# Kernel tuning notes

Hardware: AMD Instinct MI355X
Metric: run time of the kernel (lower is better)

## Reference

```python
import jax, jax.numpy as jnp
import numpy as np

DIM = 512
HEADS = 8
HEAD_DIM = DIM // HEADS
LN_EPS = 1e-5


def setup_inputs() -> dict:
    key = jax.random.key(0)
    ks = jax.random.split(key, 16)
    B, L, E = 4, 4096, DIM
    x = jax.random.normal(ks[0], (B, L, E), dtype=jnp.float32)
    w = lambda k: jax.random.normal(k, (E, E), dtype=jnp.float32) * 0.02
    b = lambda k: jax.random.normal(k, (E,), dtype=jnp.float32) * 0.02
    return {
        "x": x,
        "ln_gamma": jnp.ones((E,), jnp.float32),
        "ln_beta": jnp.zeros((E,), jnp.float32),
        "Wqr": w(ks[1]), "bqr": b(ks[2]),
        "Wqi": w(ks[3]), "bqi": b(ks[4]),
        "Wkr": w(ks[5]), "bkr": b(ks[6]),
        "Wki": w(ks[7]), "bki": b(ks[8]),
        "Wvr": w(ks[9]), "bvr": b(ks[10]),
        "Wvi": w(ks[11]), "bvi": b(ks[12]),
        "Wo": w(ks[13]),
    }


def reference(x, ln_gamma, ln_beta, Wqr, bqr, Wqi, bqi, Wkr, bkr, Wki, bki,
              Wvr, bvr, Wvi, bvi, Wo):
    B, L, E = x.shape
    H, d = HEADS, HEAD_DIM
    # LayerNorm over last dim
    mu = jnp.mean(x, axis=-1, keepdims=True)
    var = jnp.mean(jnp.square(x - mu), axis=-1, keepdims=True)
    xn = (x - mu) * jax.lax.rsqrt(var + LN_EPS) * ln_gamma + ln_beta
    # rfft along time dim -> F = L//2 + 1 frequency bins
    xf = jnp.fft.rfft(xn, axis=1, norm="ortho")
    xr, xi = jnp.real(xf), jnp.imag(xf)  # [B, F, E]
    # split real/imag QKV projections (torch Linear: y = x @ W.T + b)
    Qr = xr @ Wqr.T + bqr
    Qi = xi @ Wqi.T + bqi
    Kr = xr @ Wkr.T + bkr
    Ki = xi @ Wki.T + bki
    Vr = xr @ Wvr.T + bvr
    Vi = xi @ Wvi.T + bvi
    Fn = xr.shape[1]
    split = lambda t: t.reshape(B, Fn, H, d)  # b l (h d) -> b l h d
    Qr, Qi, Kr, Ki, Vr, Vi = map(split, (Qr, Qi, Kr, Ki, Vr, Vi))
    # scores = Qr.Kr + Qi.Ki, scaled softmax over keys
    scores = (jnp.einsum("blhd,bmhd->bhlm", Qr, Kr)
              + jnp.einsum("blhd,bmhd->bhlm", Qi, Ki))
    attn = jax.nn.softmax(scores * (d ** -0.5), axis=-1)
    out_r = jnp.einsum("bhlm,bmhd->bhld", attn, Vr)
    out_i = jnp.einsum("bhlm,bmhd->bhld", attn, Vi)
    out_f = jax.lax.complex(out_r, out_i)  # [B, H, F, d]
    out_f = jnp.transpose(out_f, (0, 2, 1, 3)).reshape(B, Fn, E)
    out_t = jnp.fft.irfft(out_f, n=L, axis=1, norm="ortho")
    return out_t @ Wo.T
```

## Files before the change

### kernel.cpp

```cpp
#include <hip/hip_runtime.h>
#include <math.h>

#define NB 4
#define NL 4096
#define NE 512
#define NH 8
#define ND 64
#define NF 2049
#define WSZ (NE * NE)

static constexpr float INV_SQRT_N = 1.0f / 64.0f;

typedef __attribute__((ext_vector_type(8))) short bf16x8;
typedef __attribute__((ext_vector_type(4))) short short4v;
typedef __attribute__((ext_vector_type(4))) float f32x4;

__device__ __forceinline__ float2 cmul(float2 a, float2 b) {
    return make_float2(a.x * b.x - a.y * b.y, a.x * b.y + a.y * b.x);
}

__device__ __forceinline__ short cvt_bf16(float f) {
    unsigned u = __float_as_uint(f);
    unsigned r = (u + 0x7FFFu + ((u >> 16) & 1u)) >> 16;
    return (short)r;
}

__device__ __forceinline__ int pack_bf16x2(float a, float b) {
    return (int)(unsigned short)cvt_bf16(a) | ((int)(unsigned short)cvt_bf16(b) << 16);
}

__device__ __forceinline__ float2 unpk(int v) {
    return make_float2(__uint_as_float(((unsigned)v & 0xffffu) << 16),
                       __uint_as_float((unsigned)v & 0xffff0000u));
}

__device__ __forceinline__ int b4rev(int t) {
    int r = __brev((unsigned)t) >> 20;
    return ((r & 0x555) << 1) | ((r & 0xAAA) >> 1);
}

__global__ __launch_bounds__(256) void twiddle_kernel(float2* __restrict__ twg) {
    int j = blockIdx.x * 256 + threadIdx.x;
    double ang = (2.0 * M_PI / (double)NL) * (double)j;
    double s, c;
    sincos(ang, &s, &c);
    twg[j] = make_float2((float)c, (float)s);
}

__global__ __launch_bounds__(256) void castw_kernel(
    const float* __restrict__ w0, const float* __restrict__ w1,
    const float* __restrict__ w2, const float* __restrict__ w3,
    const float* __restrict__ w4, const float* __restrict__ w5,
    const float* __restrict__ w6, short* __restrict__ dst) {
    int which = blockIdx.y;
    const float* s = which == 0 ? w0 : which == 1 ? w1 : which == 2 ? w2 :
                     which == 3 ? w3 : which == 4 ? w4 : which == 5 ? w5 : w6;
    long i = (long)blockIdx.x * 1024 + threadIdx.x * 4;
    float4 v = *(const float4*)(s + i);
    short4v o = {cvt_bf16(v.x), cvt_bf16(v.y), cvt_bf16(v.z), cvt_bf16(v.w)};
    *(short4v*)(dst + (long)which * WSZ + i) = o;
}

__global__ __launch_bounds__(256) void ln_kernel(
    const float* __restrict__ x, const float* __restrict__ g,
    const float* __restrict__ be, short* __restrict__ xnb) {
    int wv = threadIdx.x >> 6, lane = threadIdx.x & 63;
    long row = (long)blockIdx.x * 4 + wv;
    const float* xp = x + row * NE + lane * 8;
    float4 a = *(const float4*)xp;
    float4 b = *(const float4*)(xp + 4);
    float s  = a.x + a.y + a.z + a.w + b.x + b.y + b.z + b.w;
    float ss = a.x * a.x + a.y * a.y + a.z * a.z + a.w * a.w
             + b.x * b.x + b.y * b.y + b.z * b.z + b.w * b.w;
#pragma unroll
    for (int o = 32; o; o >>= 1) { s += __shfl_xor(s, o); ss += __shfl_xor(ss, o); }
    float mu = s * (1.0f / NE);
    float var = ss * (1.0f / NE) - mu * mu;
    float rs = rsqrtf(var + 1e-5f);
    const float* gp = g + lane * 8;
    const float* bp = be + lane * 8;
    float4 g0 = *(const float4*)gp, g1 = *(const float4*)(gp + 4);
    float4 b0 = *(const float4*)bp, b1 = *(const float4*)(bp + 4);
    bf16x8 ov;
    ov[0] = cvt_bf16((a.x - mu) * rs * g0.x + b0.x);
    ov[1] = cvt_bf16((a.y - mu) * rs * g0.y + b0.y);
    ov[2] = cvt_bf16((a.z - mu) * rs * g0.z + b0.z);
    ov[3] = cvt_bf16((a.w - mu) * rs * g0.w + b0.w);
    ov[4] = cvt_bf16((b.x - mu) * rs * g1.x + b1.x);
    ov[5] = cvt_bf16((b.y - mu) * rs * g1.y + b1.y);
    ov[6] = cvt_bf16((b.z - mu) * rs * g1.z + b1.z);
    ov[7] = cvt_bf16((b.w - mu) * rs * g1.w + b1.w);
    *(bf16x8*)(xnb + row * NE + lane * 8) = ov;
}

template <int INV>
__device__ __forceinline__ void fft4_stages(float2* sdata, const float2* tws, int tid) {
#pragma unroll
    for (int st = 0; st < 6; ++st) {
        __syncthreads();
        int Q = 1 << (2 * st);
        int tq = 10 - 2 * st;
#pragma unroll
        for (int jj = 0; jj < 4; ++jj) {
            int j = tid + jj * 256;
            int k = j & (Q - 1);
            int i0 = ((j >> (2 * st)) << (2 * st + 2)) | k;
            float2 w1 = tws[k << tq];
            float2 w2 = tws[(2 * k) << tq];
            float2 w3 = cmul(w1, w2);
            float2 a = sdata[i0];
            float2 b = cmul(w1, sdata[i0 + Q]);
            float2 c = cmul(w2, sdata[i0 + 2 * Q]);
            float2 d = cmul(w3, sdata[i0 + 3 * Q]);
            float2 t0 = make_float2(a.x + c.x, a.y + c.y);
            float2 t1 = make_float2(a.x - c.x, a.y - c.y);
            float2 t2 = make_float2(b.x + d.x, b.y + d.y);
            float2 bd = make_float2(b.x - d.x, b.y - d.y);
            float2 t3 = INV ? make_float2(-bd.y, bd.x) : make_float2(bd.y, -bd.x);
            sdata[i0]         = make_float2(t0.x + t2.x, t0.y + t2.y);
            sdata[i0 + Q]     = make_float2(t1.x + t3.x, t1.y + t3.y);
            sdata[i0 + 2 * Q] = make_float2(t0.x - t2.x, t0.y - t2.y);
            sdata[i0 + 3 * Q] = make_float2(t1.x - t3.x, t1.y - t3.y);
        }
    }
    __syncthreads();
}

__device__ __forceinline__ int ep_swizzle(int loc) {
    return ((loc & 7) << 5) | (loc >> 3);
}

__global__ __launch_bounds__(256) void rfft_pair(
    const short* __restrict__ xnb, const float2* __restrict__ twg,
    short* __restrict__ xr, short* __restrict__ xi) {
    __shared__ float2 sdata[NL];
    __shared__ float2 tws[NL / 2];
    int b = blockIdx.x >> 8;
    int e0 = ep_swizzle(blockIdx.x & 255) * 2;
    int tid = threadIdx.x;
    const short* xp = xnb + (long)b * NL * NE + e0;
#pragma unroll
    for (int jj = 0; jj < 16; ++jj) {
        int t = tid + jj * 256;
        int v = *(const int*)(xp + (long)t * NE);
        sdata[b4rev(t)] = unpk(v);
    }
#pragma unroll
    for (int jj = 0; jj < 8; ++jj) {
        int j = tid + jj * 256;
        float2 w = twg[j];
        tws[j] = make_float2(w.x, -w.y);
    }
    fft4_stages<0>(sdata, tws, tid);
    short* xrp = xr + (long)b * NF * NE + e0;
    short* xip = xi + (long)b * NF * NE + e0;
    for (int f = tid; f < NF; f += 256) {
        int M = (NL - f) & (NL - 1);
        float2 zf = sdata[f], zm = sdata[M];
        float re0 = (zf.x + zm.x) * (0.5f * INV_SQRT_N);
        float im0 = (zf.y - zm.y) * (0.5f * INV_SQRT_N);
        float re1 = (zf.y + zm.y) * (0.5f * INV_SQRT_N);
        float im1 = (zm.x - zf.x) * (0.5f * INV_SQRT_N);
        *(int*)(xrp + (long)f * NE) = pack_bf16x2(re0, re1);
        *(int*)(xip + (long)f * NE) = pack_bf16x2(im0, im1);
    }
}

__global__ __launch_bounds__(256) void irfft_pair(
    const short* __restrict__ orr, const short* __restrict__ oii,
    const float2* __restrict__ twg, short* __restrict__ yt) {
    __shared__ float2 sdata[NL];
    __shared__ float2 tws[NL / 2];
    int b = blockIdx.x >> 8;
    int e0 = ep_swizzle(blockIdx.x & 255) * 2;
    int tid = threadIdx.x;
    const short* orp = orr + (long)b * NF * NE + e0;
    const short* oip = oii + (long)b * NF * NE + e0;
    for (int f = tid; f < NF; f += 256) {
        float2 vr = unpk(*(const int*)(orp + (long)f * NE));
        float2 vi = unpk(*(const int*)(oip + (long)f * NE));
        if (f == 0 || f == NL / 2) vi = make_float2(0.f, 0.f);
        sdata[b4rev(f)] = make_float2(vr.x - vi.y, vi.x + vr.y);
        if (f > 0 && f < NL / 2) {
            sdata[b4rev(NL - f)] = make_float2(vr.x + vi.y, vr.y - vi.x);
        }
    }
#pragma unroll
    for (int jj = 0; jj < 8; ++jj) {
        int j = tid + jj * 256;
        tws[j] = twg[j];
    }
    fft4_stages<1>(sdata, tws, tid);
    short* yp = yt + (long)b * NL * NE + e0;
#pragma unroll
    for (int jj = 0; jj < 16; ++jj) {
        int t = tid + jj * 256;
        float2 z = sdata[t];
        *(int*)(yp + (long)t * NE) = pack_bf16x2(z.x * INV_SQRT_N, z.y * INV_SQRT_N);
    }
}

__device__ __forceinline__ void gemm_core(
    const short* __restrict__ A, const short* __restrict__ W,
    const float* __restrict__ bias, float scale, short* __restrict__ Cb,
    float* __restrict__ Cf, int N) {
    __shared__ short As[128][40];
    __shared__ short Bs[128][40];
    int o0 = blockIdx.x * 128;
    int n0 = blockIdx.y * 128;
    int tid = threadIdx.x;
    int lane = tid & 63, wv = tid >> 6;
    int quad = lane >> 4, cl = lane & 15;
    int rbase = (wv >> 1) << 6;
    int cbase = (wv & 1) << 6;
    int srow = tid >> 2;
    int sseg = tid & 3;
    f32x4 acc[4][4];
#pragma unroll
    for (int i = 0; i < 4; ++i)
#pragma unroll
        for (int j = 0; j < 4; ++j) acc[i][j] = (f32x4){0, 0, 0, 0};

    int ra = n0 + srow;      if (ra >= N) ra = N - 1;
    int rb = n0 + srow + 64; if (rb >= N) rb = N - 1;
    const short* Ap0 = A + (long)ra * NE + sseg * 8;
    const short* Ap1 = A + (long)rb * NE + sseg * 8;
    const short* Wp0 = W + (long)(o0 + srow) * NE + sseg * 8;
    const short* Wp1 = W + (long)(o0 + srow + 64) * NE + sseg * 8;

    bf16x8 a0 = *(const bf16x8*)Ap0, a1 = *(const bf16x8*)Ap1;
    bf16x8 b0 = *(const bf16x8*)Wp0, b1 = *(const bf16x8*)Wp1;

    for (int kt = 0; kt < 16; ++kt) {
        __syncthreads();
        *(bf16x8*)&As[srow][sseg * 8] = a0;
        *(bf16x8*)&As[srow + 64][sseg * 8] = a1;
        *(bf16x8*)&Bs[srow][sseg * 8] = b0;
        *(bf16x8*)&Bs[srow + 64][sseg * 8] = b1;
        __syncthreads();
        if (kt < 15) {
            int ko = (kt + 1) * 32;
            a0 = *(const bf16x8*)(Ap0 + ko);
            a1 = *(const bf16x8*)(Ap1 + ko);
            b0 = *(const bf16x8*)(Wp0 + ko);
            b1 = *(const bf16x8*)(Wp1 + ko);
        }
        bf16x8 ar[4], br[4];
#pragma unroll
        for (int i = 0; i < 4; ++i) ar[i] = *(const bf16x8*)&As[rbase + 16 * i + cl][quad * 8];
#pragma unroll
        for (int j = 0; j < 4; ++j) br[j] = *(const bf16x8*)&Bs[cbase + 16 * j + cl][quad * 8];
#pragma unroll
        for (int i = 0; i < 4; ++i)
#pragma unroll
            for (int j = 0; j < 4; ++j)
                acc[i][j] = __builtin_amdgcn_mfma_f32_16x16x32_bf16(ar[i], br[j], acc[i][j], 0, 0, 0);
    }
    float bv[4];
#pragma unroll
    for (int j = 0; j < 4; ++j) bv[j] = bias ? bias[o0 + cbase + 16 * j + cl] : 0.0f;
#pragma unroll
    for (int i = 0; i < 4; ++i) {
#pragma unroll
        for (int r = 0; r < 4; ++r) {
            int n = n0 + rbase + 16 * i + quad * 4 + r;
            if (n >= N) continue;
#pragma unroll
            for (int j = 0; j < 4; ++j) {
                float v = (acc[i][j][r] + bv[j]) * scale;
                int o = o0 + cbase + 16 * j + cl;
                if (Cb) Cb[(long)n * NE + o] = cvt_bf16(v);
                else    Cf[(long)n * NE + o] = v;
            }
        }
    }
}

__global__ __launch_bounds__(256) void gemm_qkv(
    const short* __restrict__ A,
    const short* __restrict__ W0, const short* __restrict__ W1, const short* __restrict__ W2,
    const float* __restrict__ b0, const float* __restrict__ b1, const float* __restrict__ b2,
    short* __restrict__ C0, short* __restrict__ C1, short* __restrict__ C2, int N) {
    int z = blockIdx.z;
    const short* W = z == 0 ? W0 : z == 1 ? W1 : W2;
    const float* bb = z == 0 ? b0 : z == 1 ? b1 : b2;
    short* C = z == 0 ? C0 : z == 1 ? C1 : C2;
    gemm_core(A, W, bb, z == 0 ? 0.125f : 1.0f, C, nullptr, N);
}

__global__ __launch_bounds__(256) void gemm_out(
    const short* __restrict__ A, const short* __restrict__ W,
    float* __restrict__ C, int N) {
    gemm_core(A, W, nullptr, 1.0f, nullptr, C, N);
}

__global__ __launch_bounds__(256) void fattn_mfma(
    const short* __restrict__ Qr, const short* __restrict__ Qi,
    const short* __restrict__ Kr, const short* __restrict__ Ki,
    const short* __restrict__ Vr, const short* __restrict__ Vi,
    short* __restrict__ Orb, short* __restrict__ Oib) {
    __shared__ short Ks[2][64][72];
    __shared__ short Vt[2][64][72];
    int tid = threadIdx.x;
    int wv = tid >> 6, lane = tid & 63;
    int quad = lane >> 4, cl = lane & 15;
    int h = blockIdx.y, b = blockIdx.z;
    long base = (long)b * NF * NE + h * ND;
    int qbase = blockIdx.x * 128 + wv * 32;

    int sk0 = (tid >> 4) << 2;
    int sd0 = (tid & 15) << 2;
    int g0 = tid >> 4;
    int dsw = tid & 15;

    bf16x8 qar[2][2], qai[2][2];
#pragma unroll
    for (int u = 0; u < 2; ++u) {
        int qrow = qbase + 16 * u + cl; if (qrow >= NF) qrow = NF - 1;
        const short* pr = Qr + base + (long)qrow * NE + 8 * quad;
        const short* pi = Qi + base + (long)qrow * NE + 8 * quad;
        qar[u][0] = *(const bf16x8*)pr;
        qar[u][1] = *(const bf16x8*)(pr + 32);
        qai[u][0] = *(const bf16x8*)pi;
        qai[u][1] = *(const bf16x8*)(pi + 32);
    }

    float ls[2] = {0.f, 0.f};
    f32x4 Or2[4][2], Oi2[4][2];
#pragma unroll
    for (int t = 0; t < 4; ++t)
#pragma unroll
        for (int u = 0; u < 2; ++u) {
            Or2[t][u] = (f32x4){0, 0, 0, 0};
            Oi2[t][u] = (f32x4){0, 0, 0, 0};
        }

    short4v lk0[4], lk1[4], lv0[4], lv1[4];
    const short* pKr = Kr + base + (long)sk0 * NE + sd0;
    const short* pKi = Ki + base + (long)sk0 * NE + sd0;
    const short* pVr = Vr + base + (long)sk0 * NE + sd0;
    const short* pVi = Vi + base + (long)sk0 * NE + sd0;
    const long TSTEP = (long)64 * NE;

    auto ldfull = [&]() {
#pragma unroll
        for (int kk = 0; kk < 4; ++kk) {
            long o = (long)kk * NE;
            lk0[kk] = *(const short4v*)(pKr + o);
            lk1[kk] = *(const short4v*)(pKi + o);
            lv0[kk] = *(const short4v*)(pVr + o);
            lv1[kk] = *(const short4v*)(pVi + o);
        }
        pKr += TSTEP; pKi += TSTEP; pVr += TSTEP; pVi += TSTEP;
    };
    auto ldmask = [&](int m0) {
        short4v z4 = {0, 0, 0, 0};
#pragma unroll
        for (int kk = 0; kk < 4; ++kk) {
            int mg = m0 + sk0 + kk;
            if (mg < NF) {
                long o = (long)kk * NE;
                lk0[kk] = *(const short4v*)(pKr + o);
                lk1[kk] = *(const short4v*)(pKi + o);
                lv0[kk] = *(const short4v*)(pVr + o);
                lv1[kk] = *(const short4v*)(pVi + o);
            } else { lk0[kk] = z4; lk1[kk] = z4; lv0[kk] = z4; lv1[kk] = z4; }
        }
    };
    ldfull();

    for (int kt = 0; kt < 33; ++kt) {
        int m0 = kt * 64;
        __syncthreads();
#pragma unroll
        for (int kk = 0; kk < 4; ++kk) {
            *(short4v*)&Ks[0][sk0 + kk][sd0] = lk0[kk];
            *(short4v*)&Ks[1][sk0 + kk][sd0] = lk1[kk];
        }
        {
            int cv = (g0 ^ dsw) << 2;
#pragma unroll
            for (int dd = 0; dd < 4; ++dd) {
                short4v t0 = {lv0[0][dd], lv0[1][dd], lv0[2][dd], lv0[3][dd]};
                *(short4v*)&Vt[0][sd0 + dd][cv] = t0;
                short4v t1 = {lv1[0][dd], lv1[1][dd], lv1[2][dd], lv1[3][dd]};
                *(short4v*)&Vt[1][sd0 + dd][cv] = t1;
            }
        }
        __syncthreads();
        if (kt < 31) ldfull();
        else if (kt == 31) ldmask(m0 + 64);

        f32x4 c[4][2];
        __builtin_amdgcn_s_setprio(1);
#pragma unroll
        for (int t = 0; t < 4; ++t) {
            const short* kr = &Ks[0][cl + 16 * t][8 * quad];
            const short* ki = &Ks[1][cl + 16 * t][8 * quad];
            bf16x8 k0 = *(const bf16x8*)kr;
            bf16x8 k1 = *(const bf16x8*)(kr + 32);
            bf16x8 k2 = *(const bf16x8*)ki;
            bf16x8 k3 = *(const bf16x8*)(ki + 32);
#pragma unroll
            for (int u = 0; u < 2; ++u) {
                f32x4 acc = (f32x4){0, 0, 0, 0};
                acc = __builtin_amdgcn_mfma_f32_16x16x32_bf16(k0, qar[u][0], acc, 0, 0, 0);
                acc = __builtin_amdgcn_mfma_f32_16x16x32_bf16(k1, qar[u][1], acc, 0, 0, 0);
                acc = __builtin_amdgcn_mfma_f32_16x16x32_bf16(k2, qai[u][0], acc, 0, 0, 0);
                acc = __builtin_amdgcn_mfma_f32_16x16x32_bf16(k3, qai[u][1], acc, 0, 0, 0);
                c[t][u] = acc;
            }
        }
        __builtin_amdgcn_s_setprio(0);

        short4v pb[4][2];
        if (kt < 32) {
#pragma unroll
            for (int t = 0; t < 4; ++t)
#pragma unroll
                for (int u = 0; u < 2; ++u) {
                    float p0 = __expf(c[t][u][0]);
                    float p1 = __expf(c[t][u][1]);
                    float p2 = __expf(c[t][u][2]);
                    float p3 = __expf(c[t][u][3]);
                    ls[u] += (p0 + p1) + (p2 + p3);
                    pb[t][u] = (short4v){cvt_bf16(p0), cvt_bf16(p1),
                                         cvt_bf16(p2), cvt_bf16(p3)};
                }
        } else {
#pragma unroll
            for (int t = 0; t < 4; ++t) {
                int kbase = m0 + 16 * t + quad * 4;
#pragma unroll
                for (int u = 0; u < 2; ++u) {
                    float p0 = (kbase + 0 < NF) ? __expf(c[t][u][0]) : 0.0f;
                    float p1 = (kbase + 1 < NF) ? __expf(c[t][u][1]) : 0.0f;
                    float p2 = (kbase + 2 < NF) ? __expf(c[t][u][2]) : 0.0f;
                    float p3 = (kbase + 3 < NF) ? __expf(c[t][u][3]) : 0.0f;
                    ls[u] += (p0 + p1) + (p2 + p3);
                    pb[t][u] = (short4v){cvt_bf16(p0), cvt_bf16(p1),
                                         cvt_bf16(p2), cvt_bf16(p3)};
                }
            }
        }

        __builtin_amdgcn_s_setprio(1);
#pragma unroll
        for (int nt = 0; nt < 4; ++nt) {
            int d = cl + 16 * nt;
            int dg = (d >> 2) & 15;
#pragma unroll
            for (int t = 0; t < 4; ++t) {
                int g = 4 * t + quad;
                int cv = ((g ^ dg) << 2);
                short4v va = *(const short4v*)&Vt[0][d][cv];
                short4v vb = *(const short4v*)&Vt[1][d][cv];
#pragma unroll
                for (int u = 0; u < 2; ++u) {
                    Or2[nt][u] = __builtin_amdgcn_mfma_f32_16x16x16bf16_1k(va, pb[t][u], Or2[nt][u], 0, 0, 0);
                    Oi2[nt][u] = __builtin_amdgcn_mfma_f32_16x16x16bf16_1k(vb, pb[t][u], Oi2[nt][u], 0, 0, 0);
                }
            }
        }
        __builtin_amdgcn_s_setprio(0);
    }

#pragma unroll
    for (int u = 0; u < 2; ++u) {
        float l2 = ls[u];
        l2 += __shfl_xor(l2, 16);
        l2 += __shfl_xor(l2, 32);
        float inv = 1.0f / l2;
        int q = qbase + 16 * u + cl;
        if (q < NF) {
            short* po = Orb + base + (long)q * NE;
            short* pi2 = Oib + base + (long)q * NE;
#pragma unroll
            for (int nt = 0; nt < 4; ++nt) {
                int d0 = 16 * nt + quad * 4;
                short4v so = {cvt_bf16(Or2[nt][u][0] * inv), cvt_bf16(Or2[nt][u][1] * inv),
                              cvt_bf16(Or2[nt][u][2] * inv), cvt_bf16(Or2[nt][u][3] * inv)};
                *(short4v*)(po + d0) = so;
                short4v si = {cvt_bf16(Oi2[nt][u][0] * inv), cvt_bf16(Oi2[nt][u][1] * inv),
                              cvt_bf16(Oi2[nt][u][2] * inv), cvt_bf16(Oi2[nt][u][3] * inv)};
                *(short4v*)(pi2 + d0) = si;
            }
        }
    }
}

extern "C" void kernel_launch(void* const* d_in, const int* in_sizes, int n_in,
                              void* d_out, int out_size, void* d_ws, size_t ws_size,
                              hipStream_t stream) {
    const float* x   = (const float*)d_in[0];
    const float* g   = (const float*)d_in[1];
    const float* be  = (const float*)d_in[2];
    const float* Wqr = (const float*)d_in[3];
    const float* bqr = (const float*)d_in[4];
    const float* Wqi = (const float*)d_in[5];
    const float* bqi = (const float*)d_in[6];
    const float* Wkr = (const float*)d_in[7];
    const float* bkr = (const float*)d_in[8];
    const float* Wki = (const float*)d_in[9];
    const float* bki = (const float*)d_in[10];
    const float* Wvr = (const float*)d_in[11];
    const float* bvr = (const float*)d_in[12];
    const float* Wvi = (const float*)d_in[13];
    const float* bvi = (const float*)d_in[14];
    const float* Wo  = (const float*)d_in[15];
    float* out = (float*)d_out;

    const long SZ_T = (long)NB * NL * NE;
    const long SZ_F = (long)NB * NF * NE;
    float2* twg = (float2*)d_ws;
    short* xnb = (short*)(twg + 2048);
    short* xr  = xnb + SZ_T;
    short* xi  = xr + SZ_F;
    short* Qr  = xi + SZ_F;
    short* Qi  = Qr + SZ_F;
    short* Kr  = Qi + SZ_F;
    short* Ki  = Kr + SZ_F;
    short* Vr  = Ki + SZ_F;
    short* Vi  = Vr + SZ_F;
    short* Orb = Vi + SZ_F;
    short* Oib = Orb + SZ_F;
    short* yt  = Oib + SZ_F;
    short* wb  = yt + SZ_T;

    twiddle_kernel<<<NL / 2 / 256, 256, 0, stream>>>(twg);
    castw_kernel<<<dim3(WSZ / 1024, 7), 256, 0, stream>>>(Wqr, Wqi, Wkr, Wki, Wvr, Wvi, Wo, wb);
    ln_kernel<<<NB * NL / 4, 256, 0, stream>>>(x, g, be, xnb);
    rfft_pair<<<NB * 256, 256, 0, stream>>>(xnb, twg, xr, xi);
    int Nf = NB * NF;
    dim3 gq(NE / 128, (Nf + 127) / 128, 3);
    gemm_qkv<<<gq, 256, 0, stream>>>(xr, wb + 0L * WSZ, wb + 2L * WSZ, wb + 4L * WSZ,
                                     bqr, bkr, bvr, Qr, Kr, Vr, Nf);
    gemm_qkv<<<gq, 256, 0, stream>>>(xi, wb + 1L * WSZ, wb + 3L * WSZ, wb + 5L * WSZ,
                                     bqi, bki, bvi, Qi, Ki, Vi, Nf);
    fattn_mfma<<<dim3(17, NH, NB), 256, 0, stream>>>(Qr, Qi, Kr, Ki, Vr, Vi, Orb, Oib);
    irfft_pair<<<NB * 256, 256, 0, stream>>>(Orb, Oib, twg, yt);
    gemm_out<<<dim3(NE / 128, NB * NL / 128), 256, 0, stream>>>(yt, wb + 6L * WSZ, out, NB * NL);
}
```

Measured before the change: 451.7 us.

## Split attention KV range across two blocks and combine partials in a new kernel

The attention kernel now splits the key/value sequence into two halves along grid z. Each block writes unnormalized fp32 partial outputs and row sums to workspace, and a new ocombine kernel sums the two halves, normalizes, and writes bf16. This doubles the attention grid from 544 to 1088 blocks so the GPU's CUs are better filled, and adds a launch-bounds occupancy hint. In exchange it adds extra fp32 global traffic for the partials plus one more kernel launch. Summing the partials without a max-shift matches the original, which also had no max subtraction.

```diff
diff --git a/kernel.cpp b/kernel.cpp
--- a/kernel.cpp
+++ b/kernel.cpp
@@ -8,6 +8,8 @@
 #define ND 64
 #define NF 2049
 #define WSZ (NE * NE)
+#define QPAD 2176
+#define OPSZ ((long)NB * NH * QPAD * 64)
 
 static constexpr float INV_SQRT_N = 1.0f / 64.0f;
 
@@ -294,19 +296,23 @@
     gemm_core(A, W, nullptr, 1.0f, nullptr, C, N);
 }
 
-__global__ __launch_bounds__(256) void fattn_mfma(
+__global__ __launch_bounds__(256, 4) void fattn_mfma(
     const short* __restrict__ Qr, const short* __restrict__ Qi,
     const short* __restrict__ Kr, const short* __restrict__ Ki,
     const short* __restrict__ Vr, const short* __restrict__ Vi,
-    short* __restrict__ Orb, short* __restrict__ Oib) {
+    float* __restrict__ Opr, float* __restrict__ Opi, float* __restrict__ lsp) {
     __shared__ short Ks[2][64][72];
     __shared__ short Vt[2][64][72];
     int tid = threadIdx.x;
     int wv = tid >> 6, lane = tid & 63;
     int quad = lane >> 4, cl = lane & 15;
-    int h = blockIdx.y, b = blockIdx.z;
+    int h = blockIdx.y;
+    int zz = blockIdx.z;
+    int b = zz >> 1, half = zz & 1;
     long base = (long)b * NF * NE + h * ND;
     int qbase = blockIdx.x * 128 + wv * 32;
+    int kt0 = half * 17;
+    int ktN = half ? 33 : 17;
 
     int sk0 = (tid >> 4) << 2;
     int sd0 = (tid & 15) << 2;
@@ -336,11 +342,11 @@
         }
 
     short4v lk0[4], lk1[4], lv0[4], lv1[4];
-    const short* pKr = Kr + base + (long)sk0 * NE + sd0;
-    const short* pKi = Ki + base + (long)sk0 * NE + sd0;
-    const short* pVr = Vr + base + (long)sk0 * NE + sd0;
-    const short* pVi = Vi + base + (long)sk0 * NE + sd0;
     const long TSTEP = (long)64 * NE;
+    const short* pKr = Kr + base + (long)sk0 * NE + sd0 + (long)kt0 * TSTEP;
+    const short* pKi = Ki + base + (long)sk0 * NE + sd0 + (long)kt0 * TSTEP;
+    const short* pVr = Vr + base + (long)sk0 * NE + sd0 + (long)kt0 * TSTEP;
+    const short* pVi = Vi + base + (long)sk0 * NE + sd0 + (long)kt0 * TSTEP;
 
     auto ldfull = [&]() {
 #pragma unroll
@@ -353,11 +359,11 @@
         }
         pKr += TSTEP; pKi += TSTEP; pVr += TSTEP; pVi += TSTEP;
     };
-    auto ldmask = [&](int m0) {
+    auto ldmask = [&]() {
         short4v z4 = {0, 0, 0, 0};
 #pragma unroll
         for (int kk = 0; kk < 4; ++kk) {
-            int mg = m0 + sk0 + kk;
+            int mg = 2048 + sk0 + kk;
             if (mg < NF) {
                 long o = (long)kk * NE;
                 lk0[kk] = *(const short4v*)(pKr + o);
@@ -369,8 +375,7 @@
     };
     ldfull();
 
-    for (int kt = 0; kt < 33; ++kt) {
-        int m0 = kt * 64;
+    for (int kt = kt0; kt < ktN; ++kt) {
         __syncthreads();
 #pragma unroll
         for (int kk = 0; kk < 4; ++kk) {
@@ -388,8 +393,10 @@
             }
         }
         __syncthreads();
-        if (kt < 31) ldfull();
-        else if (kt == 31) ldmask(m0 + 64);
+        if (kt + 1 < ktN) {
+            if (kt + 1 < 32) ldfull();
+            else ldmask();
+        }
 
         f32x4 c[4][2];
         __builtin_amdgcn_s_setprio(1);
@@ -430,7 +437,7 @@
         } else {
 #pragma unroll
             for (int t = 0; t < 4; ++t) {
-                int kbase = m0 + 16 * t + quad * 4;
+                int kbase = 2048 + 16 * t + quad * 4;
 #pragma unroll
                 for (int u = 0; u < 2; ++u) {
                     float p0 = (kbase + 0 < NF) ? __expf(c[t][u][0]) : 0.0f;
@@ -465,27 +472,64 @@
         __builtin_amdgcn_s_setprio(0);
     }
 
+    long ob = ((long)(half * NB + b) * NH + h) * ((long)QPAD * 64);
+    long lb = ((long)(half * NB + b) * NH + h) * QPAD;
 #pragma unroll
     for (int u = 0; u < 2; ++u) {
         float l2 = ls[u];
         l2 += __shfl_xor(l2, 16);
         l2 += __shfl_xor(l2, 32);
-        float inv = 1.0f / l2;
         int q = qbase + 16 * u + cl;
         if (q < NF) {
-            short* po = Orb + base + (long)q * NE;
-            short* pi2 = Oib + base + (long)q * NE;
+            if (quad == 0) lsp[lb + q] = l2;
+            float* pr = Opr + ob + (long)q * 64;
+            float* pi2 = Opi + ob + (long)q * 64;
 #pragma unroll
             for (int nt = 0; nt < 4; ++nt) {
                 int d0 = 16 * nt + quad * 4;
-                short4v so = {cvt_bf16(Or2[nt][u][0] * inv), cvt_bf16(Or2[nt][u][1] * inv),
-                              cvt_bf16(Or2[nt][u][2] * inv), cvt_bf16(Or2[nt][u][3] * inv)};
-                *(short4v*)(po + d0) = so;
-                short4v si = {cvt_bf16(Oi2[nt][u][0] * inv), cvt_bf16(Oi2[nt][u][1] * inv),
-                              cvt_bf16(Oi2[nt][u][2] * inv), cvt_bf16(Oi2[nt][u][3] * inv)};
-                *(short4v*)(pi2 + d0) = si;
+                *(f32x4*)(pr + d0) = Or2[nt][u];
+                *(f32x4*)(pi2 + d0) = Oi2[nt][u];
             }
         }
+    }
+}
+
+__global__ __launch_bounds__(256) void ocombine(
+    const float* __restrict__ Opr, const float* __restrict__ Opi,
+    const float* __restrict__ lsp, short* __restrict__ Orb, short* __restrict__ Oib) {
+    int h = blockIdx.y, b = blockIdx.z;
+    int tid = threadIdx.x;
+    int q = blockIdx.x * 64 + (tid >> 2);
+    int d0 = (tid & 3) * 16;
+    if (q >= NF) return;
+    long o0 = (((long)b * NH + h) * QPAD + q) * 64 + d0;
+    long o1 = ((((long)NB + b) * NH + h) * QPAD + q) * 64 + d0;
+    float l = lsp[((long)b * NH + h) * QPAD + q]
+            + lsp[(((long)NB + b) * NH + h) * QPAD + q];
+    float inv = 1.0f / l;
+    long base = (long)b * NF * NE + h * ND;
+    short* po = Orb + base + (long)q * NE + d0;
+    short* pi = Oib + base + (long)q * NE + d0;
+#pragma unroll
+    for (int part = 0; part < 2; ++part) {
+        bf16x8 vr, vi;
+#pragma unroll
+        for (int sub = 0; sub < 2; ++sub) {
+            float4 r1 = *(const float4*)(Opr + o0 + part * 8 + sub * 4);
+            float4 r2 = *(const float4*)(Opr + o1 + part * 8 + sub * 4);
+            float4 i1 = *(const float4*)(Opi + o0 + part * 8 + sub * 4);
+            float4 i2 = *(const float4*)(Opi + o1 + part * 8 + sub * 4);
+            vr[sub * 4 + 0] = cvt_bf16((r1.x + r2.x) * inv);
+            vr[sub * 4 + 1] = cvt_bf16((r1.y + r2.y) * inv);
+            vr[sub * 4 + 2] = cvt_bf16((r1.z + r2.z) * inv);
+            vr[sub * 4 + 3] = cvt_bf16((r1.w + r2.w) * inv);
+            vi[sub * 4 + 0] = cvt_bf16((i1.x + i2.x) * inv);
+            vi[sub * 4 + 1] = cvt_bf16((i1.y + i2.y) * inv);
+            vi[sub * 4 + 2] = cvt_bf16((i1.z + i2.z) * inv);
+            vi[sub * 4 + 3] = cvt_bf16((i1.w + i2.w) * inv);
+        }
+        *(bf16x8*)(po + part * 8) = vr;
+        *(bf16x8*)(pi + part * 8) = vi;
     }
 }
 
@@ -526,6 +570,9 @@
     short* Oib = Orb + SZ_F;
     short* yt  = Oib + SZ_F;
     short* wb  = yt + SZ_T;
+    float* Opr = (float*)(wb + 7L * WSZ);
+    float* Opi = Opr + 2 * OPSZ;
+    float* lsp = Opi + 2 * OPSZ;
 
     twiddle_kernel<<<NL / 2 / 256, 256, 0, stream>>>(twg);
     castw_kernel<<<dim3(WSZ / 1024, 7), 256, 0, stream>>>(Wqr, Wqi, Wkr, Wki, Wvr, Wvi, Wo, wb);
@@ -537,7 +584,8 @@
                                      bqr, bkr, bvr, Qr, Kr, Vr, Nf);
     gemm_qkv<<<gq, 256, 0, stream>>>(xi, wb + 1L * WSZ, wb + 3L * WSZ, wb + 5L * WSZ,
                                      bqi, bki, bvi, Qi, Ki, Vi, Nf);
-    fattn_mfma<<<dim3(17, NH, NB), 256, 0, stream>>>(Qr, Qi, Kr, Ki, Vr, Vi, Orb, Oib);
+    fattn_mfma<<<dim3(17, NH, NB * 2), 256, 0, stream>>>(Qr, Qi, Kr, Ki, Vr, Vi, Opr, Opi, lsp);
+    ocombine<<<dim3(33, NH, NB), 256, 0, stream>>>(Opr, Opi, lsp, Orb, Oib);
     irfft_pair<<<NB * 256, 256, 0, stream>>>(Orb, Oib, twg, yt);
     gemm_out<<<dim3(NE / 128, NB * NL / 128), 256, 0, stream>>>(yt, wb + 6L * WSZ, out, NB * NL);
 }
```

After: 856.1 us. +89.5%, slower.
